# Optimization experiments

Hardware: AMD Instinct MI355X
Metric: run time of the kernel (lower is better)

The kernel has to match this reference:

```python
import jax, jax.numpy as jnp
import numpy as np

DT = 0.042
GAMMA = 2.7
EPSILON = 4.7
T, B, N_INP, N_HID, N_OUT = 512, 256, 128, 512, 10


def setup_inputs() -> dict:
    key = jax.random.key(0)
    k1, k2, k3 = jax.random.split(key, 3)
    fan_in = N_INP + 2 * N_HID  # 1152, matches nn.Linear(n_inp+2*n_hid, n_hid)
    bound = 1.0 / np.sqrt(fan_in)
    x = jax.random.normal(k1, (T, B, N_INP), dtype=jnp.float32)
    W = jax.random.uniform(k2, (fan_in, N_HID), dtype=jnp.float32, minval=-bound, maxval=bound)
    b = jnp.zeros((N_HID,), dtype=jnp.float32)
    bound_o = 1.0 / np.sqrt(N_HID)
    Wout = jax.random.uniform(k3, (N_HID, N_OUT), dtype=jnp.float32, minval=-bound_o, maxval=bound_o)
    bout = jnp.zeros((N_OUT,), dtype=jnp.float32)
    return {"x": x, "W": W, "b": b, "Wout": Wout, "bout": bout}


def reference(x, W, b, Wout, bout):
    # x: [T, B, n_inp]; W: [n_inp+2*n_hid, n_hid]
    Bsz = x.shape[1]
    n_hid = W.shape[1]
    hy0 = jnp.zeros((Bsz, n_hid), dtype=x.dtype)
    hz0 = jnp.zeros((Bsz, n_hid), dtype=x.dtype)

    def step(carry, xt):
        hy, hz = carry
        # concat order matches torch.cat((x, hz, hy), 1)
        inp = jnp.concatenate([xt, hz, hy], axis=1)  # [B, n_inp+2*n_hid]
        pre = jnp.tanh(inp @ W + b)
        hz = hz + DT * (pre - GAMMA * hy - EPSILON * hz)
        hy = hy + DT * hz
        return (hy, hz), None

    (hy, hz), _ = jax.lax.scan(step, (hy0, hz0), x)
    output = hy @ Wout + bout  # [B, n_out]
    return output
```

## Files before the change

kernel.cpp:

```cpp
#include <hip/hip_runtime.h>

#define T_STEPS 512
#define BATCH   256
#define N_INP   128
#define N_HID   512
#define N_OUT   10

#define DT_C     0.042f
#define GAMMA_C  2.7f
#define EPS_C    4.7f

#define NWG        64
#define GROUP_WGS  8
#define WG_THREADS 512

typedef short          s16x8  __attribute__((ext_vector_type(8)));
typedef float          f32x16 __attribute__((ext_vector_type(16)));
typedef float          f32x4  __attribute__((ext_vector_type(4)));
typedef unsigned short u16x4  __attribute__((ext_vector_type(4)));
typedef unsigned long long u64;

__device__ inline unsigned short f2bf(float f) {
  union { float f; unsigned u; } v; v.f = f;
  unsigned r = v.u + 0x7fffu + ((v.u >> 16) & 1u);
  return (unsigned short)(r >> 16);
}
__device__ inline float bf2f(unsigned short h) {
  union { unsigned u; float f; } v; v.u = ((unsigned)h) << 16;
  return v.f;
}

__device__ inline void pub8(unsigned short* p, u16x4 v) {
  union { u16x4 v; u64 q; } u; u.v = v;
  __hip_atomic_store((u64*)p, u.q, __ATOMIC_RELAXED, __HIP_MEMORY_SCOPE_AGENT);
}

#define STATE_LD8(HB, HP)                                                    \
  asm volatile(                                                              \
    "global_load_dwordx4 %0, %8, off sc0 sc1\n\t"                            \
    "global_load_dwordx4 %1, %8, off offset:32 sc0 sc1\n\t"                  \
    "global_load_dwordx4 %2, %8, off offset:64 sc0 sc1\n\t"                  \
    "global_load_dwordx4 %3, %8, off offset:96 sc0 sc1\n\t"                  \
    "global_load_dwordx4 %4, %8, off offset:128 sc0 sc1\n\t"                 \
    "global_load_dwordx4 %5, %8, off offset:160 sc0 sc1\n\t"                 \
    "global_load_dwordx4 %6, %8, off offset:192 sc0 sc1\n\t"                 \
    "global_load_dwordx4 %7, %8, off offset:224 sc0 sc1\n\t"                 \
    "s_waitcnt vmcnt(0)"                                                     \
    : "=&v"(HB[0]), "=&v"(HB[1]), "=&v"(HB[2]), "=&v"(HB[3]),                \
      "=&v"(HB[4]), "=&v"(HB[5]), "=&v"(HB[6]), "=&v"(HB[7])                 \
    : "v"(HP)                                                                \
    : "memory")

__global__ __launch_bounds__(WG_THREADS, 2) void cornn_kernel(
    const float* __restrict__ x, const float* __restrict__ W,
    const float* __restrict__ bias, unsigned short* __restrict__ Hbf,
    float* __restrict__ Hy32, unsigned* __restrict__ flags_ws) {
  const int tid   = threadIdx.x;
  const int lane  = tid & 63;
  const int ks    = tid >> 6;
  const int half  = lane >> 5;
  const int half8 = half << 3;
  const int lcol  = lane & 31;
  const int mi    = blockIdx.x & 7;
  const int ni    = blockIdx.x >> 3;
  const int rowA  = (mi << 5) + lcol;

  unsigned* gflags = flags_ws + mi * 64;

  __shared__ float sC[8][2048];
  __shared__ float sB[64];

  s16x8 whi0[8], wlo0[8], whi1[8], wlo1[8];
  s16x8 wxhi0, wxlo0, wxhi1, wxlo1;
  const int c0t = (ni << 6) + lcol;
  const int c1t = c0t + 32;
  #pragma unroll
  for (int i = 0; i < 8; ++i) {
    const int wr = 128 + (ks << 7) + i * 16 + half8;
    const float* wp0 = W + (size_t)wr * N_HID + c0t;
    s16x8 hi0, lo0, hi1, lo1;
    #pragma unroll
    for (int j = 0; j < 8; ++j) {
      float f0 = wp0[(size_t)j * N_HID];
      float f1 = wp0[(size_t)j * N_HID + 32];
      unsigned short h0 = f2bf(f0), h1 = f2bf(f1);
      hi0[j] = (short)h0;  lo0[j] = (short)f2bf(f0 - bf2f(h0));
      hi1[j] = (short)h1;  lo1[j] = (short)f2bf(f1 - bf2f(h1));
    }
    whi0[i] = hi0; wlo0[i] = lo0; whi1[i] = hi1; wlo1[i] = lo1;
  }
  {
    const int wr = (ks << 4) + half8;
    const float* wp0 = W + (size_t)wr * N_HID + c0t;
    s16x8 hi0, lo0, hi1, lo1;
    #pragma unroll
    for (int j = 0; j < 8; ++j) {
      float f0 = wp0[(size_t)j * N_HID];
      float f1 = wp0[(size_t)j * N_HID + 32];
      unsigned short h0 = f2bf(f0), h1 = f2bf(f1);
      hi0[j] = (short)h0;  lo0[j] = (short)f2bf(f0 - bf2f(h0));
      hi1[j] = (short)h1;  lo1[j] = (short)f2bf(f1 - bf2f(h1));
    }
    wxhi0 = hi0; wxlo0 = lo0; wxhi1 = hi1; wxlo1 = lo1;
  }
  if (tid < 64) sB[tid] = bias[(ni << 6) + tid];

  const int e0   = tid << 2;
  const int rowL = e0 >> 6, c0 = e0 & 63;
  const int rowG = (mi << 5) + rowL;
  const int colG = (ni << 6) + c0;
  f32x4 hz = {0.f, 0.f, 0.f, 0.f};
  f32x4 hy = {0.f, 0.f, 0.f, 0.f};

  const unsigned short* hb2[2];
  hb2[0] = Hbf + (size_t)rowA * 1024 + (ks << 7) + half8;
  hb2[1] = hb2[0] + 256 * 1024;
  unsigned short* wz[2];
  unsigned short* wy[2];
  wz[0] = Hbf + (size_t)rowG * 1024 + colG;       wz[1] = wz[0] + 256 * 1024;
  wy[0] = wz[0] + 512;                            wy[1] = wz[1] + 512;

  __syncthreads();

  for (int t = 0; t < T_STEPS; ++t) {
    f32x16 acc0 = {};
    f32x16 acc1 = {};

    {
      const float* xp = x + (size_t)t * (BATCH * N_INP) + (size_t)rowA * N_INP
                        + (ks << 4) + half8;
      f32x4 a0 = *reinterpret_cast<const f32x4*>(xp);
      f32x4 a1 = *reinterpret_cast<const f32x4*>(xp + 4);
      s16x8 ahi, alo;
      #pragma unroll
      for (int j = 0; j < 4; ++j) {
        float f0 = a0[j], f1 = a1[j];
        unsigned short h0 = f2bf(f0), h1 = f2bf(f1);
        ahi[j]     = (short)h0;  ahi[j + 4] = (short)h1;
        alo[j]     = (short)f2bf(f0 - bf2f(h0));
        alo[j + 4] = (short)f2bf(f1 - bf2f(h1));
      }
      acc0 = __builtin_amdgcn_mfma_f32_32x32x16_bf16(ahi, wxhi0, acc0, 0, 0, 0);
      acc0 = __builtin_amdgcn_mfma_f32_32x32x16_bf16(ahi, wxlo0, acc0, 0, 0, 0);
      acc0 = __builtin_amdgcn_mfma_f32_32x32x16_bf16(alo, wxhi0, acc0, 0, 0, 0);
      acc1 = __builtin_amdgcn_mfma_f32_32x32x16_bf16(ahi, wxhi1, acc1, 0, 0, 0);
      acc1 = __builtin_amdgcn_mfma_f32_32x32x16_bf16(ahi, wxlo1, acc1, 0, 0, 0);
      acc1 = __builtin_amdgcn_mfma_f32_32x32x16_bf16(alo, wxhi1, acc1, 0, 0, 0);
    }

    if (t > 0) {
      const unsigned ep = (unsigned)t;
      const int l = lane & 7;
      for (;;) {
        unsigned v = __hip_atomic_load(&gflags[l], __ATOMIC_RELAXED, __HIP_MEMORY_SCOPE_AGENT);
        if (__ballot((lane >= 8) | (l == ni) | (v >= ep)) == ~0ull) break;
        __builtin_amdgcn_s_sleep(2);
      }

      const unsigned short* hp = hb2[t & 1];
      f32x4 hbuf[8];
      STATE_LD8(hbuf, hp);
      #pragma unroll
      for (int i = 0; i < 8; ++i) {
        union { f32x4 f; s16x8 s; } u; u.f = hbuf[i];
        acc0 = __builtin_amdgcn_mfma_f32_32x32x16_bf16(u.s, whi0[i], acc0, 0, 0, 0);
        acc0 = __builtin_amdgcn_mfma_f32_32x32x16_bf16(u.s, wlo0[i], acc0, 0, 0, 0);
        acc1 = __builtin_amdgcn_mfma_f32_32x32x16_bf16(u.s, whi1[i], acc1, 0, 0, 0);
        acc1 = __builtin_amdgcn_mfma_f32_32x32x16_bf16(u.s, wlo1[i], acc1, 0, 0, 0);
      }
    }

    #pragma unroll
    for (int r = 0; r < 16; ++r) {
      const int rowL_r = (r & 3) + ((r >> 2) << 3) + (half << 2);
      sC[ks][rowL_r * 64 + lcol]      = acc0[r];
      sC[ks][rowL_r * 64 + 32 + lcol] = acc1[r];
    }
    __syncthreads();

    {
      f32x4 s = *reinterpret_cast<f32x4*>(&sC[0][e0]);
      #pragma unroll
      for (int w = 1; w < 8; ++w) s += *reinterpret_cast<f32x4*>(&sC[w][e0]);
      u16x4 pz, py;
      #pragma unroll
      for (int j = 0; j < 4; ++j) {
        float pre = tanhf(s[j] + sB[c0 + j]);
        float z = hz[j] + DT_C * (pre - GAMMA_C * hy[j] - EPS_C * hz[j]);
        float y = hy[j] + DT_C * z;
        hz[j] = z; hy[j] = y;
        pz[j] = f2bf(z); py[j] = f2bf(y);
      }
      const int wb = (t & 1) ^ 1;
      pub8(wz[wb], pz);
      pub8(wy[wb], py);
    }
    __syncthreads();
    if (tid == 0)
      __hip_atomic_store(&gflags[ni], (unsigned)t + 1u, __ATOMIC_RELAXED, __HIP_MEMORY_SCOPE_AGENT);
  }

  if (Hy32 != nullptr)
    *reinterpret_cast<f32x4*>(Hy32 + (size_t)rowG * 512 + colG) = hy;
}

__global__ void cornn_out_kernel(const float* __restrict__ Hy32,
                                 const unsigned short* __restrict__ HbfFinal,
                                 const float* __restrict__ Wout,
                                 const float* __restrict__ bout,
                                 float* __restrict__ out) {
  const int b = blockIdx.x;
  const int lane = threadIdx.x;
  float a[N_OUT];
  #pragma unroll
  for (int c = 0; c < N_OUT; ++c) a[c] = 0.f;
  #pragma unroll
  for (int j = 0; j < 8; ++j) {
    const int k = lane + (j << 6);
    const float h = Hy32 ? Hy32[(size_t)b * N_HID + k]
                         : bf2f(HbfFinal[(size_t)b * 1024 + 512 + k]);
    const float* wr = Wout + (size_t)k * N_OUT;
    #pragma unroll
    for (int c = 0; c < N_OUT; ++c) a[c] += h * wr[c];
  }
  #pragma unroll
  for (int c = 0; c < N_OUT; ++c) {
    float v = a[c];
    for (int off = 32; off > 0; off >>= 1) v += __shfl_down(v, off, 64);
    if (lane == 0) out[(size_t)b * N_OUT + c] = v + bout[c];
  }
}

extern "C" void kernel_launch(void* const* d_in, const int* in_sizes, int n_in,
                              void* d_out, int out_size, void* d_ws, size_t ws_size,
                              hipStream_t stream) {
  (void)in_sizes; (void)n_in; (void)out_size;
  const float* x    = (const float*)d_in[0];
  const float* W    = (const float*)d_in[1];
  const float* bias = (const float*)d_in[2];
  const float* Wout = (const float*)d_in[3];
  const float* bout = (const float*)d_in[4];

  char* ws = (char*)d_ws;
  unsigned*       flags = (unsigned*)ws;
  unsigned short* Hbf   = (unsigned short*)(ws + 4096);
  float*          Hy32  = (float*)(ws + 4096 + (size_t)2 * 256 * 1024 * 2);
  const size_t needed = 4096 + (size_t)2 * 256 * 1024 * 2 + (size_t)256 * 512 * 4;
  float* hyPtr = (ws_size >= needed) ? Hy32 : nullptr;

  hipMemsetAsync(flags, 0, 4096, stream);

  cornn_kernel<<<dim3(NWG), dim3(WG_THREADS), 0, stream>>>(x, W, bias, Hbf, hyPtr, flags);

  cornn_out_kernel<<<dim3(BATCH), dim3(64), 0, stream>>>(hyPtr, Hbf, Wout, bout,
                                                         (float*)d_out);
}
```

Before: 2.285 ms.

## Use per-wave flags with pipelined polling and prefetch next-step inputs

Result: slower. 2.978 ms (+30.4%).

```diff
diff --git a/kernel.cpp b/kernel.cpp
--- a/kernel.cpp
+++ b/kernel.cpp
@@ -11,7 +11,6 @@
 #define EPS_C    4.7f
 
 #define NWG        64
-#define GROUP_WGS  8
 #define WG_THREADS 512
 
 typedef short          s16x8  __attribute__((ext_vector_type(8)));
@@ -65,7 +64,7 @@
   const int ni    = blockIdx.x >> 3;
   const int rowA  = (mi << 5) + lcol;
 
-  unsigned* gflags = flags_ws + mi * 64;
+  unsigned* gflags = flags_ws + mi * 128;
 
   __shared__ float sC[8][2048];
   __shared__ float sB[64];
@@ -73,7 +72,6 @@
   s16x8 whi0[8], wlo0[8], whi1[8], wlo1[8];
   s16x8 wxhi0, wxlo0, wxhi1, wxlo1;
   const int c0t = (ni << 6) + lcol;
-  const int c1t = c0t + 32;
   #pragma unroll
   for (int i = 0; i < 8; ++i) {
     const int wr = 128 + (ks << 7) + i * 16 + half8;
@@ -120,6 +118,15 @@
   wz[0] = Hbf + (size_t)rowG * 1024 + colG;       wz[1] = wz[0] + 256 * 1024;
   wy[0] = wz[0] + 512;                            wy[1] = wz[1] + 512;
 
+  const int pl = lane & 15;
+  const unsigned* fpoll = gflags + (2 * (ks & 3) + (pl >> 3)) * 8 + (pl & 7);
+  const bool plane = (lane >= 16);
+  unsigned* myflag = gflags + ni * 8 + ks;
+
+  const float* xbase = x + (size_t)rowA * N_INP + (ks << 4) + half8;
+  f32x4 xa0 = *reinterpret_cast<const f32x4*>(xbase);
+  f32x4 xa1 = *reinterpret_cast<const f32x4*>(xbase + 4);
+
   __syncthreads();
 
   for (int t = 0; t < T_STEPS; ++t) {
@@ -127,14 +134,10 @@
     f32x16 acc1 = {};
 
     {
-      const float* xp = x + (size_t)t * (BATCH * N_INP) + (size_t)rowA * N_INP
-                        + (ks << 4) + half8;
-      f32x4 a0 = *reinterpret_cast<const f32x4*>(xp);
-      f32x4 a1 = *reinterpret_cast<const f32x4*>(xp + 4);
       s16x8 ahi, alo;
       #pragma unroll
       for (int j = 0; j < 4; ++j) {
-        float f0 = a0[j], f1 = a1[j];
+        float f0 = xa0[j], f1 = xa1[j];
         unsigned short h0 = f2bf(f0), h1 = f2bf(f1);
         ahi[j]     = (short)h0;  ahi[j + 4] = (short)h1;
         alo[j]     = (short)f2bf(f0 - bf2f(h0));
@@ -150,11 +153,20 @@
 
     if (t > 0) {
       const unsigned ep = (unsigned)t;
-      const int l = lane & 7;
+      unsigned v0, v1;
+      asm volatile("global_load_dword %0, %1, off sc0 sc1"
+                   : "=v"(v0) : "v"(fpoll) : "memory");
+      asm volatile("global_load_dword %0, %1, off sc0 sc1"
+                   : "=v"(v1) : "v"(fpoll) : "memory");
       for (;;) {
-        unsigned v = __hip_atomic_load(&gflags[l], __ATOMIC_RELAXED, __HIP_MEMORY_SCOPE_AGENT);
-        if (__ballot((lane >= 8) | (l == ni) | (v >= ep)) == ~0ull) break;
-        __builtin_amdgcn_s_sleep(2);
+        asm volatile("s_waitcnt vmcnt(1)" : "+v"(v0) :: "memory");
+        if (__ballot(plane | (v0 >= ep)) == ~0ull) break;
+        asm volatile("global_load_dword %0, %1, off sc0 sc1"
+                     : "=v"(v0) : "v"(fpoll) : "memory");
+        asm volatile("s_waitcnt vmcnt(1)" : "+v"(v1) :: "memory");
+        if (__ballot(plane | (v1 >= ep)) == ~0ull) break;
+        asm volatile("global_load_dword %0, %1, off sc0 sc1"
+                     : "=v"(v1) : "v"(fpoll) : "memory");
       }
 
       const unsigned short* hp = hb2[t & 1];
@@ -170,6 +182,13 @@
       }
     }
 
+    {
+      const int tn = (t < T_STEPS - 1) ? t + 1 : t;
+      const float* xp = xbase + (size_t)tn * (BATCH * N_INP);
+      xa0 = *reinterpret_cast<const f32x4*>(xp);
+      xa1 = *reinterpret_cast<const f32x4*>(xp + 4);
+    }
+
     #pragma unroll
     for (int r = 0; r < 16; ++r) {
       const int rowL_r = (r & 3) + ((r >> 2) << 3) + (half << 2);
@@ -178,10 +197,12 @@
     }
     __syncthreads();
 
+    f32x4 s = *reinterpret_cast<f32x4*>(&sC[0][e0]);
+    #pragma unroll
+    for (int w = 1; w < 8; ++w) s += *reinterpret_cast<f32x4*>(&sC[w][e0]);
+    __syncthreads();
+
     {
-      f32x4 s = *reinterpret_cast<f32x4*>(&sC[0][e0]);
-      #pragma unroll
-      for (int w = 1; w < 8; ++w) s += *reinterpret_cast<f32x4*>(&sC[w][e0]);
       u16x4 pz, py;
       #pragma unroll
       for (int j = 0; j < 4; ++j) {
@@ -195,9 +216,9 @@
       pub8(wz[wb], pz);
       pub8(wy[wb], py);
     }
-    __syncthreads();
-    if (tid == 0)
-      __hip_atomic_store(&gflags[ni], (unsigned)t + 1u, __ATOMIC_RELAXED, __HIP_MEMORY_SCOPE_AGENT);
+    asm volatile("s_waitcnt vmcnt(0)" ::: "memory");
+    if (lane == 0)
+      __hip_atomic_store(myflag, (unsigned)t + 1u, __ATOMIC_RELAXED, __HIP_MEMORY_SCOPE_AGENT);
   }
 
   if (Hy32 != nullptr)
```
